# Kernel optimization log

Measured on AMD Instinct MI355X. Metric: run time of the kernel, lower is better.

## Reference

```python
import jax, jax.numpy as jnp
import numpy as np

H, N, M = 1024, 128, 512
EPS_COS = 1e-8


def setup_inputs() -> dict:
    key = jax.random.key(0)
    ks = iter(jax.random.split(key, 64))
    def rn(shape, s=0.02):
        return jax.random.normal(next(ks), shape, jnp.float32) * s
    x = jax.random.normal(next(ks), (1, H), jnp.float32)
    prw = jax.random.uniform(next(ks), (1, N), jnp.float32)
    prev_read_w = prw / jnp.sum(prw, axis=1, keepdims=True)
    pww = jax.random.uniform(next(ks), (1, N), jnp.float32)
    prev_write_w = pww / jnp.sum(pww, axis=1, keepdims=True)
    inp = {
        "x": x,
        "prev_read_w": prev_read_w,
        "prev_write_w": prev_write_w,
        "h0": rn((1, H), 0.1),
        "c0": rn((1, H), 0.1),
        "memory": jnp.ones((N, M), jnp.float32),
        "W_ih": rn((4 * H, H)), "W_hh": rn((4 * H, H)),
        "b_ih": rn((4 * H,)), "b_hh": rn((4 * H,)),
        "rk_w": rn((M, H)), "rk_b": rn((M,)),
        "rbeta_w": rn((1, H)), "rbeta_b": rn((1,)),
        "rg_w": rn((1, H)), "rg_b": rn((1,)),
        "rs_w": rn((N, H)), "rs_b": rn((N,)),
        "rgamma_w": rn((1, H)), "rgamma_b": rn((1,)),
        "wk_w": rn((M, H)), "wk_b": rn((M,)),
        "wbeta_w": rn((1, H)), "wbeta_b": rn((1,)),
        "wg_w": rn((1, H)), "wg_b": rn((1,)),
        "ws_w": rn((N, H)), "ws_b": rn((N,)),
        "wgamma_w": rn((1, H)), "wgamma_b": rn((1,)),
        "we_w": rn((N * M, H)), "we_b": rn((N * M,)),
        "wa_w": rn((M, H)), "wa_b": rn((M,)),
        "fc_w": rn((H, H + M)), "fc_b": rn((H,)),
    }
    return inp


def _lstm_cell(x, h, c, W_ih, W_hh, b_ih, b_hh):
    # torch gate order: i, f, g, o
    gates = x @ W_ih.T + b_ih + h @ W_hh.T + b_hh  # (1, 4H)
    i, f, g, o = jnp.split(gates, 4, axis=1)
    c_new = jax.nn.sigmoid(f) * c + jax.nn.sigmoid(i) * jnp.tanh(g)
    h_new = jax.nn.sigmoid(o) * jnp.tanh(c_new)
    return h_new, c_new


def _address(x, prev_w, mem, k_w, k_b, beta_w, beta_b, g_w, g_b, s_w, s_b, gamma_w, gamma_b):
    k = x @ k_w.T + k_b                                  # (1, M)
    beta = jax.nn.softplus(x @ beta_w.T + beta_b)        # (1, 1)
    g = jax.nn.sigmoid(x @ g_w.T + g_b)                  # (1, 1)
    s = jax.nn.softmax(x @ s_w.T + s_b, axis=-1)         # (1, N)
    gamma = 1.0 + jax.nn.softplus(x @ gamma_w.T + gamma_b)  # (1, 1)
    # cosine similarity of each memory row with k
    mem_n = jnp.maximum(jnp.linalg.norm(mem, axis=1), EPS_COS)     # (N,)
    k_n = jnp.maximum(jnp.linalg.norm(k[0]), EPS_COS)
    cos = (mem @ k[0]) / (mem_n * k_n)                   # (N,)
    w_c = jax.nn.softmax(beta * cos[None, :], axis=1)    # (1, N)
    w_g = g * w_c + (1.0 - g) * prev_w                   # (1, N)
    # circular convolution: w_t[i] = sum_j w_g[j] * s[(i - j) mod N]
    idx = (jnp.arange(N)[:, None] - jnp.arange(N)[None, :]) % N    # (N, N)
    w_t = (s[0][idx] @ w_g[0])[None, :]                  # (1, N)
    w = w_t ** gamma
    w = w / (jnp.sum(w, axis=1, keepdims=True) + 1e-16)
    return w


def reference(x, prev_read_w, prev_write_w, h0, c0, memory,
              W_ih, W_hh, b_ih, b_hh,
              rk_w, rk_b, rbeta_w, rbeta_b, rg_w, rg_b, rs_w, rs_b, rgamma_w, rgamma_b,
              wk_w, wk_b, wbeta_w, wbeta_b, wg_w, wg_b, ws_w, ws_b, wgamma_w, wgamma_b,
              we_w, we_b, wa_w, wa_b, fc_w, fc_b):
    sg = jax.lax.stop_gradient
    # controller (single LSTM step, batch 1)
    h, c = _lstm_cell(x, h0, c0, W_ih, W_hh, b_ih, b_hh)
    co = h  # controller output (1, H)
    mem = sg(memory)  # memory is detached in the original
    # read head
    rw = _address(co, prev_read_w, mem, rk_w, rk_b, rbeta_w, rbeta_b,
                  rg_w, rg_b, rs_w, rs_b, rgamma_w, rgamma_b)
    read = rw @ mem                                      # (1, M)
    # write head (note: receives prev_read_w, faithful to source)
    ww = _address(co, prev_read_w, mem, wk_w, wk_b, wbeta_w, wbeta_b,
                  wg_w, wg_b, ws_w, ws_b, wgamma_w, wgamma_b)
    e = jax.nn.sigmoid(co @ we_w.T + we_b)               # (1, N*M)
    a = co @ wa_w.T + wa_b                               # (1, M)
    # memory write with detached w, e, a (as in original)
    ww_d, e_d, a_d = sg(ww), sg(e), sg(a)
    new_mem = memory * (1.0 - ww_d @ e_d.reshape(N, M))  # (1,M) broadcast over (N,M)
    new_mem = new_mem + ww_d.T * a_d                     # (N,1)*(1,M)
    # output projection
    fc_in = jnp.concatenate([co, read], axis=1)          # (1, H+M)
    out = fc_in @ fc_w.T + fc_b                          # (1, H)
    return (out, sg(rw), sg(ww), h, c, new_mem)
```

## Files before the change

kernel.cpp:

```cpp
#include <hip/hip_runtime.h>
#include <math.h>

#define HH 1024
#define NN 128
#define MM 512

#define OFF_RW 1024
#define OFF_WW 1152
#define OFF_H  1280
#define OFF_C  2304
#define OFF_NM 3328

#define WS_GATES   0
#define WS_CO      4096
#define WS_MNORM   5120
#define WS_E       5248
#define WS_A       70784
#define WS_KR      71296
#define WS_KW      71808
#define WS_RSLOG   72320
#define WS_WSLOG   72448
#define WS_FCPART  72576
#define WS_SCAL    73600
#define WS_RWV     73608
#define WS_WWV     73736
#define WS_ERASE   73864
#define WS_READ    74376

__device__ __forceinline__ float sigmoidf_(float z) { return 1.f / (1.f + expf(-z)); }
__device__ __forceinline__ float softplusf_(float z) {
    return fmaxf(z, 0.f) + log1pf(expf(-fabsf(z)));
}
__device__ __forceinline__ float wave_reduce(float v) {
    #pragma unroll
    for (int off = 32; off > 0; off >>= 1) v += __shfl_down(v, off, 64);
    return v;
}

__global__ __launch_bounds__(256) void k1_gates_norms(
    const float* __restrict__ x, const float* __restrict__ h0,
    const float* __restrict__ W_ih, const float* __restrict__ W_hh,
    const float* __restrict__ b_ih, const float* __restrict__ b_hh,
    const float* __restrict__ memory, float* __restrict__ gates,
    float* __restrict__ mem_norm)
{
    int t = threadIdx.x, lane = t & 63, wv = t >> 6;
    if (blockIdx.x < 1024) {
        int r = blockIdx.x * 4 + wv;
        const float4* wi = (const float4*)(W_ih + (long long)r * HH);
        const float4* wh = (const float4*)(W_hh + (long long)r * HH);
        const float4* x4 = (const float4*)x;
        const float4* h4 = (const float4*)h0;
        float acc = 0.f;
        #pragma unroll
        for (int q = 0; q < 4; ++q) {
            float4 aa = wi[q * 64 + lane], bb = x4[q * 64 + lane];
            acc += aa.x * bb.x + aa.y * bb.y + aa.z * bb.z + aa.w * bb.w;
        }
        #pragma unroll
        for (int q = 0; q < 4; ++q) {
            float4 aa = wh[q * 64 + lane], bb = h4[q * 64 + lane];
            acc += aa.x * bb.x + aa.y * bb.y + aa.z * bb.z + aa.w * bb.w;
        }
        acc = wave_reduce(acc);
        if (lane == 0) gates[r] = acc + b_ih[r] + b_hh[r];
    } else {
        int n = (blockIdx.x - 1024) * 4 + wv;
        const float4* r4 = (const float4*)(memory + n * MM);
        float acc = 0.f;
        #pragma unroll
        for (int q = 0; q < 2; ++q) {
            float4 aa = r4[q * 64 + lane];
            acc += aa.x * aa.x + aa.y * aa.y + aa.z * aa.z + aa.w * aa.w;
        }
        acc = wave_reduce(acc);
        if (lane == 0) mem_norm[n] = sqrtf(acc);
    }
}

__global__ __launch_bounds__(256) void k2_lstm(
    const float* __restrict__ gates, const float* __restrict__ c0,
    float* __restrict__ out, float* __restrict__ co)
{
    int j = blockIdx.x * 256 + threadIdx.x;
    float gi = gates[j], gf = gates[j + 1024], gg = gates[j + 2048], go = gates[j + 3072];
    float cn = sigmoidf_(gf) * c0[j] + sigmoidf_(gi) * tanhf(gg);
    float hn = sigmoidf_(go) * tanhf(cn);
    out[OFF_H + j] = hn;
    out[OFF_C + j] = cn;
    co[j] = hn;
}

#define K3_ROWS 68358
__global__ __launch_bounds__(256) void k3_gemvs(
    const float* __restrict__ co,
    const float* __restrict__ we_w, const float* __restrict__ we_b,
    const float* __restrict__ wa_w, const float* __restrict__ wa_b,
    const float* __restrict__ rk_w, const float* __restrict__ rk_b,
    const float* __restrict__ wk_w, const float* __restrict__ wk_b,
    const float* __restrict__ rs_w, const float* __restrict__ rs_b,
    const float* __restrict__ sw_w, const float* __restrict__ sw_b,
    const float* __restrict__ fc_w, const float* __restrict__ fc_b,
    const float* __restrict__ rbeta_w, const float* __restrict__ rbeta_b,
    const float* __restrict__ rg_w, const float* __restrict__ rg_b,
    const float* __restrict__ rgamma_w, const float* __restrict__ rgamma_b,
    const float* __restrict__ wbeta_w, const float* __restrict__ wbeta_b,
    const float* __restrict__ wg_w, const float* __restrict__ wg_b,
    const float* __restrict__ wgamma_w, const float* __restrict__ wgamma_b,
    float* __restrict__ e, float* __restrict__ a,
    float* __restrict__ kr, float* __restrict__ kw,
    float* __restrict__ rs_logit, float* __restrict__ ws_logit,
    float* __restrict__ fc_part, float* __restrict__ scal)
{
    int t = threadIdx.x, lane = t & 63, wv = t >> 6;
    long long r = (long long)blockIdx.x * 4 + wv;
    if (r >= K3_ROWS) return;
    const float* row;
    float bias = 0.f;
    float* dst;
    bool sig = false;
    if (r < 65536) {
        row = we_w + r * HH; if (lane == 0) bias = we_b[r]; dst = e + r; sig = true;
    } else if (r < 66048) {
        int i = (int)(r - 65536); row = wa_w + (long long)i * HH; if (lane == 0) bias = wa_b[i]; dst = a + i;
    } else if (r < 66560) {
        int i = (int)(r - 66048); row = rk_w + (long long)i * HH; if (lane == 0) bias = rk_b[i]; dst = kr + i;
    } else if (r < 67072) {
        int i = (int)(r - 66560); row = wk_w + (long long)i * HH; if (lane == 0) bias = wk_b[i]; dst = kw + i;
    } else if (r < 67200) {
        int i = (int)(r - 67072); row = rs_w + (long long)i * HH; if (lane == 0) bias = rs_b[i]; dst = rs_logit + i;
    } else if (r < 67328) {
        int i = (int)(r - 67200); row = sw_w + (long long)i * HH; if (lane == 0) bias = sw_b[i]; dst = ws_logit + i;
    } else if (r < 68352) {
        int i = (int)(r - 67328); row = fc_w + (long long)i * 1536; if (lane == 0) bias = fc_b[i]; dst = fc_part + i;
    } else {
        int i = (int)(r - 68352);
        const float* wsrc; const float* bsrc;
        switch (i) {
            case 0: wsrc = rbeta_w;  bsrc = rbeta_b;  break;
            case 1: wsrc = rg_w;     bsrc = rg_b;     break;
            case 2: wsrc = rgamma_w; bsrc = rgamma_b; break;
            case 3: wsrc = wbeta_w;  bsrc = wbeta_b;  break;
            case 4: wsrc = wg_w;     bsrc = wg_b;     break;
            default: wsrc = wgamma_w; bsrc = wgamma_b; break;
        }
        row = wsrc; if (lane == 0) bias = bsrc[0]; dst = scal + i;
    }
    const float4* r4 = (const float4*)row;
    const float4* c4 = (const float4*)co;
    float acc = 0.f;
    #pragma unroll
    for (int q = 0; q < 4; ++q) {
        float4 aa = r4[q * 64 + lane], bb = c4[q * 64 + lane];
        acc += aa.x * bb.x + aa.y * bb.y + aa.z * bb.z + aa.w * bb.w;
    }
    acc = wave_reduce(acc);
    if (lane == 0) {
        float vv = acc + bias;
        if (sig) vv = sigmoidf_(vv);
        *dst = vv;
    }
}

__global__ __launch_bounds__(256) void k4_address(
    const float* __restrict__ kr, const float* __restrict__ kw,
    const float* __restrict__ scal,
    const float* __restrict__ rs_logit, const float* __restrict__ ws_logit,
    const float* __restrict__ prev_w, const float* __restrict__ mem_norm,
    const float* __restrict__ memory,
    float* __restrict__ out, float* __restrict__ rwv, float* __restrict__ wwv)
{
    int head = blockIdx.x;
    int t = threadIdx.x, lane = t & 63, wv = t >> 6;
    const float* k = head ? kw : kr;
    const float* slog = head ? ws_logit : rs_logit;
    float beta  = softplusf_(scal[head ? 3 : 0]);
    float gg    = sigmoidf_(scal[head ? 4 : 1]);
    float gamma = 1.f + softplusf_(scal[head ? 5 : 2]);

    __shared__ float tmp[256];
    __shared__ float s_cos[128];
    __shared__ float s_s[128];
    __shared__ float s_wg[128];

    float a0 = k[t], a1 = k[t + 256];
    tmp[t] = a0 * a0 + a1 * a1;
    __syncthreads();
    for (int off = 128; off > 0; off >>= 1) { if (t < off) tmp[t] += tmp[t + off]; __syncthreads(); }
    float k_norm = tmp[0];
    __syncthreads();
    k_norm = sqrtf(k_norm);

    for (int i = 0; i < 32; ++i) {
        int n = wv * 32 + i;
        const float4* r4 = (const float4*)(memory + n * MM);
        const float4* k4 = (const float4*)k;
        float acc = 0.f;
        #pragma unroll
        for (int q = 0; q < 2; ++q) {
            float4 aa = r4[q * 64 + lane], bb = k4[q * 64 + lane];
            acc += aa.x * bb.x + aa.y * bb.y + aa.z * bb.z + aa.w * bb.w;
        }
        acc = wave_reduce(acc);
        if (lane == 0)
            s_cos[n] = acc / (fmaxf(mem_norm[n], 1e-8f) * fmaxf(k_norm, 1e-8f));
    }
    __syncthreads();

    float z = (t < 128) ? beta * s_cos[t] : -1e30f;
    tmp[t] = z; __syncthreads();
    for (int off = 128; off > 0; off >>= 1) { if (t < off) tmp[t] = fmaxf(tmp[t], tmp[t + off]); __syncthreads(); }
    float zmax = tmp[0]; __syncthreads();
    float ez = (t < 128) ? expf(z - zmax) : 0.f;
    tmp[t] = ez; __syncthreads();
    for (int off = 128; off > 0; off >>= 1) { if (t < off) tmp[t] += tmp[t + off]; __syncthreads(); }
    float zsum = tmp[0]; __syncthreads();
    if (t < 128) s_wg[t] = gg * (ez / zsum) + (1.f - gg) * prev_w[t];

    float sl = (t < 128) ? slog[t] : -1e30f;
    tmp[t] = sl; __syncthreads();
    for (int off = 128; off > 0; off >>= 1) { if (t < off) tmp[t] = fmaxf(tmp[t], tmp[t + off]); __syncthreads(); }
    float smax = tmp[0]; __syncthreads();
    float es = (t < 128) ? expf(sl - smax) : 0.f;
    tmp[t] = es; __syncthreads();
    for (int off = 128; off > 0; off >>= 1) { if (t < off) tmp[t] += tmp[t + off]; __syncthreads(); }
    float ssum = tmp[0]; __syncthreads();
    if (t < 128) s_s[t] = es / ssum;
    __syncthreads();

    float wt = 0.f;
    if (t < 128) {
        #pragma unroll 8
        for (int j = 0; j < 128; ++j) wt += s_wg[j] * s_s[(t - j) & 127];
        wt = powf(wt, gamma);
    }
    tmp[t] = (t < 128) ? wt : 0.f;
    __syncthreads();
    for (int off = 128; off > 0; off >>= 1) { if (t < off) tmp[t] += tmp[t + off]; __syncthreads(); }
    float wsum = tmp[0]; __syncthreads();
    if (t < 128) {
        float wf = wt / (wsum + 1e-16f);
        out[(head ? OFF_WW : OFF_RW) + t] = wf;
        (head ? wwv : rwv)[t] = wf;
    }
}

__global__ __launch_bounds__(256) void k5a_contract(
    const float* __restrict__ e, const float* __restrict__ memory,
    const float* __restrict__ wwv, const float* __restrict__ rwv,
    float* __restrict__ erase, float* __restrict__ readv)
{
    int b = blockIdx.x, t = threadIdx.x;
    if (b < 2) {
        int m = b * 256 + t;
        float acc = 0.f;
        for (int n = 0; n < 128; ++n) acc += wwv[n] * e[n * MM + m];
        erase[m] = acc;
    } else {
        int m = (b - 2) * 256 + t;
        float acc = 0.f;
        for (int n = 0; n < 128; ++n) acc += rwv[n] * memory[n * MM + m];
        readv[m] = acc;
    }
}

__global__ __launch_bounds__(256) void k5b_final(
    const float* __restrict__ memory, const float* __restrict__ erase,
    const float* __restrict__ wwv, const float* __restrict__ a,
    const float* __restrict__ fc_w, const float* __restrict__ fc_part,
    const float* __restrict__ readv, float* __restrict__ out)
{
    int b = blockIdx.x, t = threadIdx.x;
    if (b < 256) {
        int idx = b * 256 + t;
        int n = idx >> 9, m = idx & 511;
        out[OFF_NM + idx] = memory[idx] * (1.f - erase[m]) + wwv[n] * a[m];
    } else {
        int w = (b - 256) * 4 + (t >> 6);
        int lane = t & 63;
        const float4* r4 = (const float4*)(fc_w + (long long)w * 1536 + 1024);
        const float4* v4 = (const float4*)readv;
        float acc = 0.f;
        #pragma unroll
        for (int q = 0; q < 2; ++q) {
            float4 aa = r4[q * 64 + lane], bb = v4[q * 64 + lane];
            acc += aa.x * bb.x + aa.y * bb.y + aa.z * bb.z + aa.w * bb.w;
        }
        acc = wave_reduce(acc);
        if (lane == 0) out[w] = fc_part[w] + acc;
    }
}

extern "C" void kernel_launch(void* const* d_in, const int* in_sizes, int n_in,
                              void* d_out, int out_size, void* d_ws, size_t ws_size,
                              hipStream_t stream)
{
    const float* x           = (const float*)d_in[0];
    const float* prev_read_w = (const float*)d_in[1];
    const float* h0      = (const float*)d_in[3];
    const float* c0      = (const float*)d_in[4];
    const float* memory  = (const float*)d_in[5];
    const float* W_ih    = (const float*)d_in[6];
    const float* W_hh    = (const float*)d_in[7];
    const float* b_ih    = (const float*)d_in[8];
    const float* b_hh    = (const float*)d_in[9];
    const float* rk_w    = (const float*)d_in[10];
    const float* rk_b    = (const float*)d_in[11];
    const float* rbeta_w = (const float*)d_in[12];
    const float* rbeta_b = (const float*)d_in[13];
    const float* rg_w    = (const float*)d_in[14];
    const float* rg_b    = (const float*)d_in[15];
    const float* rs_w    = (const float*)d_in[16];
    const float* rs_b    = (const float*)d_in[17];
    const float* rgamma_w = (const float*)d_in[18];
    const float* rgamma_b = (const float*)d_in[19];
    const float* wk_w    = (const float*)d_in[20];
    const float* wk_b    = (const float*)d_in[21];
    const float* wbeta_w = (const float*)d_in[22];
    const float* wbeta_b = (const float*)d_in[23];
    const float* wg_w    = (const float*)d_in[24];
    const float* wg_b    = (const float*)d_in[25];
    const float* sw_w    = (const float*)d_in[26];
    const float* sw_b    = (const float*)d_in[27];
    const float* wgamma_w = (const float*)d_in[28];
    const float* wgamma_b = (const float*)d_in[29];
    const float* we_w    = (const float*)d_in[30];
    const float* we_b    = (const float*)d_in[31];
    const float* wa_w    = (const float*)d_in[32];
    const float* wa_b    = (const float*)d_in[33];
    const float* fc_w    = (const float*)d_in[34];
    const float* fc_b    = (const float*)d_in[35];

    float* ws  = (float*)d_ws;
    float* out = (float*)d_out;

    float* gates    = ws + WS_GATES;
    float* co       = ws + WS_CO;
    float* mem_norm = ws + WS_MNORM;
    float* e        = ws + WS_E;
    float* a        = ws + WS_A;
    float* kr       = ws + WS_KR;
    float* kw       = ws + WS_KW;
    float* rs_logit = ws + WS_RSLOG;
    float* ws_logit = ws + WS_WSLOG;
    float* fc_part  = ws + WS_FCPART;
    float* scal     = ws + WS_SCAL;
    float* rwv      = ws + WS_RWV;
    float* wwv      = ws + WS_WWV;
    float* erase    = ws + WS_ERASE;
    float* readv    = ws + WS_READ;

    k1_gates_norms<<<1056, 256, 0, stream>>>(x, h0, W_ih, W_hh, b_ih, b_hh,
                                             memory, gates, mem_norm);
    k2_lstm<<<4, 256, 0, stream>>>(gates, c0, out, co);
    k3_gemvs<<<(K3_ROWS + 3) / 4, 256, 0, stream>>>(
        co, we_w, we_b, wa_w, wa_b, rk_w, rk_b, wk_w, wk_b, rs_w, rs_b,
        sw_w, sw_b, fc_w, fc_b,
        rbeta_w, rbeta_b, rg_w, rg_b, rgamma_w, rgamma_b,
        wbeta_w, wbeta_b, wg_w, wg_b, wgamma_w, wgamma_b,
        e, a, kr, kw, rs_logit, ws_logit, fc_part, scal);
    k4_address<<<2, 256, 0, stream>>>(kr, kw, scal, rs_logit, ws_logit,
                                      prev_read_w, mem_norm, memory,
                                      out, rwv, wwv);
    k5a_contract<<<4, 256, 0, stream>>>(e, memory, wwv, rwv, erase, readv);
    k5b_final<<<512, 256, 0, stream>>>(memory, erase, wwv, a, fc_w, fc_part,
                                       readv, out);
}
```

Before: 495.7 us.

## Fuse erase GEMV with weighted contraction via atomics; fold read into address kernel

The large we_w GEMV now runs after addressing, so each wave computes two sigmoid erase values and atomically accumulates ww[n]*e into the erase vector. This removes the 256KB e buffer round trip and the serial contraction kernel. The read-vector contraction moves into the read-head block of the address kernel, and erase is zeroed in the LSTM kernel. The cost is many float atomics onto only 512 addresses, plus a nondeterministic summation order.

```diff
diff --git a/kernel.cpp b/kernel.cpp
--- a/kernel.cpp
+++ b/kernel.cpp
@@ -14,18 +14,16 @@
 #define WS_GATES   0
 #define WS_CO      4096
 #define WS_MNORM   5120
-#define WS_E       5248
-#define WS_A       70784
-#define WS_KR      71296
-#define WS_KW      71808
-#define WS_RSLOG   72320
-#define WS_WSLOG   72448
-#define WS_FCPART  72576
-#define WS_SCAL    73600
-#define WS_RWV     73608
-#define WS_WWV     73736
-#define WS_ERASE   73864
-#define WS_READ    74376
+#define WS_A       5248
+#define WS_KR      5760
+#define WS_KW      6272
+#define WS_RSLOG   6784
+#define WS_WSLOG   6912
+#define WS_FCPART  7040
+#define WS_SCAL    8064
+#define WS_WWV     8072
+#define WS_ERASE   8200
+#define WS_READ    8712
 
 __device__ __forceinline__ float sigmoidf_(float z) { return 1.f / (1.f + expf(-z)); }
 __device__ __forceinline__ float softplusf_(float z) {
@@ -80,7 +78,7 @@
 
 __global__ __launch_bounds__(256) void k2_lstm(
     const float* __restrict__ gates, const float* __restrict__ c0,
-    float* __restrict__ out, float* __restrict__ co)
+    float* __restrict__ out, float* __restrict__ co, float* __restrict__ erase)
 {
     int j = blockIdx.x * 256 + threadIdx.x;
     float gi = gates[j], gf = gates[j + 1024], gg = gates[j + 2048], go = gates[j + 3072];
@@ -89,12 +87,12 @@
     out[OFF_H + j] = hn;
     out[OFF_C + j] = cn;
     co[j] = hn;
-}
-
-#define K3_ROWS 68358
-__global__ __launch_bounds__(256) void k3_gemvs(
+    if (j < 512) erase[j] = 0.f;
+}
+
+#define K3S_ROWS 2822
+__global__ __launch_bounds__(256) void k3_small(
     const float* __restrict__ co,
-    const float* __restrict__ we_w, const float* __restrict__ we_b,
     const float* __restrict__ wa_w, const float* __restrict__ wa_b,
     const float* __restrict__ rk_w, const float* __restrict__ rk_b,
     const float* __restrict__ wk_w, const float* __restrict__ wk_b,
@@ -107,34 +105,30 @@
     const float* __restrict__ wbeta_w, const float* __restrict__ wbeta_b,
     const float* __restrict__ wg_w, const float* __restrict__ wg_b,
     const float* __restrict__ wgamma_w, const float* __restrict__ wgamma_b,
-    float* __restrict__ e, float* __restrict__ a,
-    float* __restrict__ kr, float* __restrict__ kw,
+    float* __restrict__ a, float* __restrict__ kr, float* __restrict__ kw,
     float* __restrict__ rs_logit, float* __restrict__ ws_logit,
     float* __restrict__ fc_part, float* __restrict__ scal)
 {
     int t = threadIdx.x, lane = t & 63, wv = t >> 6;
-    long long r = (long long)blockIdx.x * 4 + wv;
-    if (r >= K3_ROWS) return;
+    int r = blockIdx.x * 4 + wv;
+    if (r >= K3S_ROWS) return;
     const float* row;
     float bias = 0.f;
     float* dst;
-    bool sig = false;
-    if (r < 65536) {
-        row = we_w + r * HH; if (lane == 0) bias = we_b[r]; dst = e + r; sig = true;
-    } else if (r < 66048) {
-        int i = (int)(r - 65536); row = wa_w + (long long)i * HH; if (lane == 0) bias = wa_b[i]; dst = a + i;
-    } else if (r < 66560) {
-        int i = (int)(r - 66048); row = rk_w + (long long)i * HH; if (lane == 0) bias = rk_b[i]; dst = kr + i;
-    } else if (r < 67072) {
-        int i = (int)(r - 66560); row = wk_w + (long long)i * HH; if (lane == 0) bias = wk_b[i]; dst = kw + i;
-    } else if (r < 67200) {
-        int i = (int)(r - 67072); row = rs_w + (long long)i * HH; if (lane == 0) bias = rs_b[i]; dst = rs_logit + i;
-    } else if (r < 67328) {
-        int i = (int)(r - 67200); row = sw_w + (long long)i * HH; if (lane == 0) bias = sw_b[i]; dst = ws_logit + i;
-    } else if (r < 68352) {
-        int i = (int)(r - 67328); row = fc_w + (long long)i * 1536; if (lane == 0) bias = fc_b[i]; dst = fc_part + i;
+    if (r < 512) {
+        row = wa_w + (long long)r * HH; if (lane == 0) bias = wa_b[r]; dst = a + r;
+    } else if (r < 1024) {
+        int i = r - 512; row = rk_w + (long long)i * HH; if (lane == 0) bias = rk_b[i]; dst = kr + i;
+    } else if (r < 1536) {
+        int i = r - 1024; row = wk_w + (long long)i * HH; if (lane == 0) bias = wk_b[i]; dst = kw + i;
+    } else if (r < 1664) {
+        int i = r - 1536; row = rs_w + (long long)i * HH; if (lane == 0) bias = rs_b[i]; dst = rs_logit + i;
+    } else if (r < 1792) {
+        int i = r - 1664; row = sw_w + (long long)i * HH; if (lane == 0) bias = sw_b[i]; dst = ws_logit + i;
+    } else if (r < 2816) {
+        int i = r - 1792; row = fc_w + (long long)i * 1536; if (lane == 0) bias = fc_b[i]; dst = fc_part + i;
     } else {
-        int i = (int)(r - 68352);
+        int i = r - 2816;
         const float* wsrc; const float* bsrc;
         switch (i) {
             case 0: wsrc = rbeta_w;  bsrc = rbeta_b;  break;
@@ -155,11 +149,7 @@
         acc += aa.x * bb.x + aa.y * bb.y + aa.z * bb.z + aa.w * bb.w;
     }
     acc = wave_reduce(acc);
-    if (lane == 0) {
-        float vv = acc + bias;
-        if (sig) vv = sigmoidf_(vv);
-        *dst = vv;
-    }
+    if (lane == 0) *dst = acc + bias;
 }
 
 __global__ __launch_bounds__(256) void k4_address(
@@ -168,7 +158,7 @@
     const float* __restrict__ rs_logit, const float* __restrict__ ws_logit,
     const float* __restrict__ prev_w, const float* __restrict__ mem_norm,
     const float* __restrict__ memory,
-    float* __restrict__ out, float* __restrict__ rwv, float* __restrict__ wwv)
+    float* __restrict__ out, float* __restrict__ wwv, float* __restrict__ readv)
 {
     int head = blockIdx.x;
     int t = threadIdx.x, lane = t & 63, wv = t >> 6;
@@ -182,14 +172,14 @@
     __shared__ float s_cos[128];
     __shared__ float s_s[128];
     __shared__ float s_wg[128];
+    __shared__ float s_w[128];
 
     float a0 = k[t], a1 = k[t + 256];
     tmp[t] = a0 * a0 + a1 * a1;
     __syncthreads();
     for (int off = 128; off > 0; off >>= 1) { if (t < off) tmp[t] += tmp[t + off]; __syncthreads(); }
-    float k_norm = tmp[0];
-    __syncthreads();
-    k_norm = sqrtf(k_norm);
+    float k_norm = sqrtf(tmp[0]);
+    __syncthreads();
 
     for (int i = 0; i < 32; ++i) {
         int n = wv * 32 + i;
@@ -241,30 +231,54 @@
     if (t < 128) {
         float wf = wt / (wsum + 1e-16f);
         out[(head ? OFF_WW : OFF_RW) + t] = wf;
-        (head ? wwv : rwv)[t] = wf;
-    }
-}
-
-__global__ __launch_bounds__(256) void k5a_contract(
-    const float* __restrict__ e, const float* __restrict__ memory,
-    const float* __restrict__ wwv, const float* __restrict__ rwv,
-    float* __restrict__ erase, float* __restrict__ readv)
-{
-    int b = blockIdx.x, t = threadIdx.x;
-    if (b < 2) {
-        int m = b * 256 + t;
-        float acc = 0.f;
-        for (int n = 0; n < 128; ++n) acc += wwv[n] * e[n * MM + m];
-        erase[m] = acc;
-    } else {
-        int m = (b - 2) * 256 + t;
-        float acc = 0.f;
-        for (int n = 0; n < 128; ++n) acc += rwv[n] * memory[n * MM + m];
-        readv[m] = acc;
-    }
-}
-
-__global__ __launch_bounds__(256) void k5b_final(
+        s_w[t] = wf;
+        if (head) wwv[t] = wf;
+    }
+    __syncthreads();
+
+    if (head == 0) {
+        for (int m = t; m < MM; m += 256) {
+            float acc = 0.f;
+            #pragma unroll 4
+            for (int n = 0; n < NN; ++n) acc += s_w[n] * memory[n * MM + m];
+            readv[m] = acc;
+        }
+    }
+}
+
+__global__ __launch_bounds__(256) void k5_bige(
+    const float* __restrict__ co,
+    const float* __restrict__ we_w, const float* __restrict__ we_b,
+    const float* __restrict__ wwv, float* __restrict__ erase)
+{
+    int t = threadIdx.x, lane = t & 63, wv = t >> 6;
+    int wid = blockIdx.x * 4 + wv;
+    long long r0 = (long long)wid * 2;
+    const float4* w0 = (const float4*)(we_w + r0 * HH);
+    const float4* w1 = (const float4*)(we_w + (r0 + 1) * HH);
+    const float4* c4 = (const float4*)co;
+    float acc0 = 0.f, acc1 = 0.f;
+    #pragma unroll
+    for (int q = 0; q < 4; ++q) {
+        float4 bb = c4[q * 64 + lane];
+        float4 a0 = w0[q * 64 + lane];
+        float4 a1 = w1[q * 64 + lane];
+        acc0 += a0.x * bb.x + a0.y * bb.y + a0.z * bb.z + a0.w * bb.w;
+        acc1 += a1.x * bb.x + a1.y * bb.y + a1.z * bb.z + a1.w * bb.w;
+    }
+    acc0 = wave_reduce(acc0);
+    acc1 = wave_reduce(acc1);
+    if (lane == 0) {
+        int n0 = (int)(r0 >> 9), m0 = (int)(r0 & 511);
+        float e0 = sigmoidf_(acc0 + we_b[r0]);
+        float e1 = sigmoidf_(acc1 + we_b[r0 + 1]);
+        atomicAdd(&erase[m0], wwv[n0] * e0);
+        int n1 = (int)((r0 + 1) >> 9), m1 = (int)((r0 + 1) & 511);
+        atomicAdd(&erase[m1], wwv[n1] * e1);
+    }
+}
+
+__global__ __launch_bounds__(256) void k6_final(
     const float* __restrict__ memory, const float* __restrict__ erase,
     const float* __restrict__ wwv, const float* __restrict__ a,
     const float* __restrict__ fc_w, const float* __restrict__ fc_part,
@@ -337,7 +351,6 @@
     float* gates    = ws + WS_GATES;
     float* co       = ws + WS_CO;
     float* mem_norm = ws + WS_MNORM;
-    float* e        = ws + WS_E;
     float* a        = ws + WS_A;
     float* kr       = ws + WS_KR;
     float* kw       = ws + WS_KW;
@@ -345,24 +358,23 @@
     float* ws_logit = ws + WS_WSLOG;
     float* fc_part  = ws + WS_FCPART;
     float* scal     = ws + WS_SCAL;
-    float* rwv      = ws + WS_RWV;
     float* wwv      = ws + WS_WWV;
     float* erase    = ws + WS_ERASE;
     float* readv    = ws + WS_READ;
 
     k1_gates_norms<<<1056, 256, 0, stream>>>(x, h0, W_ih, W_hh, b_ih, b_hh,
                                              memory, gates, mem_norm);
-    k2_lstm<<<4, 256, 0, stream>>>(gates, c0, out, co);
-    k3_gemvs<<<(K3_ROWS + 3) / 4, 256, 0, stream>>>(
-        co, we_w, we_b, wa_w, wa_b, rk_w, rk_b, wk_w, wk_b, rs_w, rs_b,
-        sw_w, sw_b, fc_w, fc_b,
+    k2_lstm<<<4, 256, 0, stream>>>(gates, c0, out, co, erase);
+    k3_small<<<(K3S_ROWS + 3) / 4, 256, 0, stream>>>(
+        co, wa_w, wa_b, rk_w, rk_b, wk_w, wk_b, rs_w, rs_b, sw_w, sw_b,
+        fc_w, fc_b,
         rbeta_w, rbeta_b, rg_w, rg_b, rgamma_w, rgamma_b,
         wbeta_w, wbeta_b, wg_w, wg_b, wgamma_w, wgamma_b,
-        e, a, kr, kw, rs_logit, ws_logit, fc_part, scal);
+        a, kr, kw, rs_logit, ws_logit, fc_part, scal);
     k4_address<<<2, 256, 0, stream>>>(kr, kw, scal, rs_logit, ws_logit,
                                       prev_read_w, mem_norm, memory,
-                                      out, rwv, wwv);
-    k5a_contract<<<4, 256, 0, stream>>>(e, memory, wwv, rwv, erase, readv);
-    k5b_final<<<512, 256, 0, stream>>>(memory, erase, wwv, a, fc_w, fc_part,
-                                       readv, out);
-}
+                                      out, wwv, readv);
+    k5_bige<<<8192, 256, 0, stream>>>(co, we_w, we_b, wwv, erase);
+    k6_final<<<512, 256, 0, stream>>>(memory, erase, wwv, a, fc_w, fc_part,
+                                      readv, out);
+}
```

Measured after the change: 496.4 us. No clear change (+0.1%).
